# Performance work log

Measured on AMD Instinct MI355X. Metric: run time of the kernel, lower is better.

The kernel has to match this reference:

```python
import jax, jax.numpy as jnp
import numpy as np

B, D, C, T, DEPTH = 4096, 1024, 1000, 32, 6
N_INTERNAL = 2 ** DEPTH - 1
N_LEAVES = 2 ** DEPTH


def setup_inputs() -> dict:
    key = jax.random.key(0)
    k0, k1, k2 = jax.random.split(key, 3)
    x = jax.random.normal(k0, (B, D), jnp.float32)
    split_weights = jax.random.normal(k1, (T, N_INTERNAL, D), jnp.float32) * 0.1
    split_biases = jnp.zeros((T, N_INTERNAL), jnp.float32)
    leaf_logits = jax.random.normal(k2, (T, N_LEAVES, C), jnp.float32) * 0.1
    tree_weights = jnp.ones((T,), jnp.float32) / T
    log_temperature = jnp.zeros((), jnp.float32)
    return {
        "x": x,
        "split_weights": split_weights,
        "split_biases": split_biases,
        "leaf_logits": leaf_logits,
        "tree_weights": tree_weights,
        "log_temperature": log_temperature,
    }


def reference(x, split_weights, split_biases, leaf_logits, tree_weights, log_temperature):
    depth = int(np.log2(leaf_logits.shape[1]))
    temp = jnp.clip(jnp.exp(log_temperature), 0.1, 5.0)
    # split probabilities for all trees at once: [B, T, I]
    logits = jnp.einsum('bd,tid->bti', x, split_weights) + split_biases[None, :, :]
    s = jax.nn.sigmoid(logits / temp)
    b, t, _ = s.shape
    # iterative-doubling path probabilities; BFS leaf order matches the
    # original per-leaf loop (left child multiplies (1-s), right multiplies s)
    mu = jnp.ones((b, t, 1), s.dtype)
    for d in range(depth):
        lvl = s[:, :, 2 ** d - 1: 2 ** (d + 1) - 1]  # [B, T, 2^d] level-d splits
        mu = jnp.stack([mu * (1.0 - lvl), mu * lvl], axis=-1).reshape(b, t, 2 ** (d + 1))
    leaf_class_probs = jax.nn.softmax(leaf_logits / temp, axis=-1)  # [T, L, C]
    w = jax.nn.softmax(tree_weights, axis=0)                        # [T]
    # fused tree-weighted blend, avoids materializing [B, T, C]
    return jnp.einsum('btl,t,tlc->bc', mu, w, leaf_class_probs)
```

## Files before the change

kernel.cpp:

```cpp
#include <hip/hip_runtime.h>
#include <cstdint>
#include <cstddef>

constexpr int Bv = 4096;
constexpr int Dv = 1024;
constexpr int Cv = 1000;
constexpr int Tv = 32;
constexpr int NI = 63;
constexpr int NL = 64;
constexpr int TNp = 2048;
constexpr int TL = Tv * NL;
constexpr int Npad = 1024;

typedef _Float16 h8  __attribute__((ext_vector_type(8)));
typedef _Float16 h4  __attribute__((ext_vector_type(4)));
typedef short    s8v __attribute__((ext_vector_type(8)));
typedef unsigned short us8 __attribute__((ext_vector_type(8)));
typedef float    f4v __attribute__((ext_vector_type(4)));

constexpr size_t N_X    = (size_t)Bv * Dv;
constexpr size_t N_W    = (size_t)TNp * Dv;
constexpr size_t OFF_XH = 64;
constexpr size_t OFF_WH = OFF_XH + N_X / 2;
constexpr size_t OFF_P  = OFF_WH + N_W / 2;
constexpr size_t OFF_MH = OFF_P + (size_t)TL * Cv;
constexpr size_t OFF_PTH= OFF_MH + (size_t)Bv * TL / 2;

__device__ __forceinline__ unsigned short f2bf_rn(float x) {
    unsigned u = __float_as_uint(x);
    return (unsigned short)((u + 0x7fffu + ((u >> 16) & 1u)) >> 16);
}

__device__ __forceinline__ void gll16(const void* gptr, void* lptr) {
    __builtin_amdgcn_global_load_lds(
        (const __attribute__((address_space(1))) unsigned int*)gptr,
        (__attribute__((address_space(3))) unsigned int*)lptr,
        16, 0, 0);
}

__global__ __launch_bounds__(256)
void k_prep(const float* __restrict__ x, const float* __restrict__ sw,
            _Float16* __restrict__ Xh, _Float16* __restrict__ Wh) {
    const int b = blockIdx.x;
    const int tid = threadIdx.x;
    const int nbx = (int)(N_X / 1024);
    if (b < nbx) {
        const size_t i4 = ((size_t)b * 256 + tid) * 4;
        const float4 v = *reinterpret_cast<const float4*>(&x[i4]);
        h4 vh;
        vh[0] = (_Float16)v.x; vh[1] = (_Float16)v.y;
        vh[2] = (_Float16)v.z; vh[3] = (_Float16)v.w;
        *reinterpret_cast<h4*>(&Xh[i4]) = vh;
    } else {
        const size_t d4 = ((size_t)(b - nbx) * 256 + tid) * 4;
        const int row = (int)(d4 >> 10);
        const int col = (int)(d4 & 1023);
        const int t = row >> 6, i = row & 63;
        float4 v = make_float4(0.f, 0.f, 0.f, 0.f);
        if (i < NI)
            v = *reinterpret_cast<const float4*>(&sw[(size_t)(t * NI + i) * Dv + col]);
        h4 vh;
        vh[0] = (_Float16)v.x; vh[1] = (_Float16)v.y;
        vh[2] = (_Float16)v.z; vh[3] = (_Float16)v.w;
        *reinterpret_cast<h4*>(&Wh[d4]) = vh;
    }
}

__global__ __launch_bounds__(256, 2)
void k_gemm1mu(const _Float16* __restrict__ Xh, const _Float16* __restrict__ Wh,
               const float* __restrict__ bias, const float* __restrict__ tw,
               const float* __restrict__ lt, unsigned short* __restrict__ MH) {
    __shared__ __align__(16) char lds[4 * 64 * 65 * 4];

    const int tid = threadIdx.x;
    const int wg  = (blockIdx.x & 7) * 64 + (blockIdx.x >> 3);
    const int blk = wg >> 6;
    const int j   = wg & 63;
    const int bx  = (blk & 3) * 4 + (j & 3);
    const int by  = (blk >> 2) * 16 + (j >> 2);
    const int bm = by * 128, bn = bx * 128;

    const int lane = tid & 63, wv = tid >> 6;
    const int wr = wv >> 1, wc = wv & 1;
    const int lrow = lane & 15, kg = (lane >> 4) * 8;
    const int sr = lane >> 2, sc = (lane & 3) * 8;

    const float temp = fminf(fmaxf(expf(lt[0]), 0.1f), 5.0f);
    const float invT = 1.0f / temp;
    const int mytree = 2 * bx + wc;
    float wm = -3.4e38f;
    #pragma unroll
    for (int t = 0; t < Tv; ++t) wm = fmaxf(wm, tw[t]);
    float wsum = 0.f, wmine = 0.f;
    #pragma unroll
    for (int t = 0; t < Tv; ++t) {
        const float e = expf(tw[t] - wm);
        wsum += e;
        if (t == mytree) wmine = e;
    }
    const float wt = wmine / wsum;

    f4v acc[4][4] = {};

#define STG(bufi, k0)                                                         \
    { _Pragma("unroll")                                                       \
      for (int i_ = 0; i_ < 2; ++i_) {                                        \
        const int ch_  = wv * 2 + i_;                                         \
        const int row_ = ch_ * 16 + sr;                                       \
        gll16(&Xh[(size_t)(bm + row_) * Dv + (k0) + sc],                      \
              lds + (bufi) * 16384 + ch_ * 1024);                             \
        gll16(&Wh[(size_t)(bn + row_) * Dv + (k0) + sc],                      \
              lds + (bufi) * 16384 + 8192 + ch_ * 1024);                      \
      } }

    STG(0, 0);
    for (int t = 0; t < 32; ++t) {
        const int cur = t & 1;
        if (t < 31) {
            STG(cur ^ 1, (t + 1) * 32);
            asm volatile("s_waitcnt vmcnt(4)" ::: "memory");
        } else {
            asm volatile("s_waitcnt vmcnt(0)" ::: "memory");
        }
        __builtin_amdgcn_s_barrier();
        __builtin_amdgcn_sched_barrier(0);

        h8 a[4], b[4];
        #pragma unroll
        for (int mf = 0; mf < 4; ++mf)
            a[mf] = *reinterpret_cast<const h8*>(
                lds + cur * 16384 + (wr * 64 + mf * 16 + lrow) * 64 + kg * 2);
        #pragma unroll
        for (int nf = 0; nf < 4; ++nf)
            b[nf] = *reinterpret_cast<const h8*>(
                lds + cur * 16384 + 8192 + (wc * 64 + nf * 16 + lrow) * 64 + kg * 2);
        #pragma unroll
        for (int mf = 0; mf < 4; ++mf)
            #pragma unroll
            for (int nf = 0; nf < 4; ++nf)
                acc[mf][nf] = __builtin_amdgcn_mfma_f32_16x16x32_f16(a[mf], b[nf], acc[mf][nf], 0, 0, 0);

        __builtin_amdgcn_sched_barrier(0);
        asm volatile("s_waitcnt lgkmcnt(0)" ::: "memory");
        __builtin_amdgcn_s_barrier();
    }
#undef STG

    float* scr = (float*)lds + wv * (64 * 65);
    #pragma unroll
    for (int nf = 0; nf < 4; ++nf) {
        const int colB = nf * 16 + lrow;
        const int gcol = bn + wc * 64 + colB;
        const int ii = gcol & 63;
        const float bv = (ii < NI) ? bias[(gcol >> 6) * NI + ii] : 0.f;
        #pragma unroll
        for (int mf = 0; mf < 4; ++mf) {
            #pragma unroll
            for (int r = 0; r < 4; ++r) {
                const int rowB = mf * 16 + (lane >> 4) * 4 + r;
                const float z = (acc[mf][nf][r] + bv) * invT;
                scr[rowB * 65 + colB] = 1.0f / (1.0f + __expf(-z));
            }
        }
    }
    asm volatile("s_waitcnt lgkmcnt(0)" ::: "memory");

    const float* srow = scr + lane * 65;
    float mu[NL];
    mu[0] = wt;
    #pragma unroll
    for (int d = 0; d < 6; ++d) {
        const int width = 1 << d;
        #pragma unroll
        for (int i = width - 1; i >= 0; --i) {
            const float sv = srow[width - 1 + i];
            const float m  = mu[i];
            mu[2 * i + 1] = m * sv;
            mu[2 * i]     = m * (1.0f - sv);
        }
    }
    const size_t obase = (size_t)(bm + wr * 64 + lane) * TL + (size_t)mytree * 64;
    #pragma unroll
    for (int c = 0; c < 8; ++c) {
        us8 vh;
        #pragma unroll
        for (int jj = 0; jj < 8; ++jj) vh[jj] = f2bf_rn(mu[c * 8 + jj]);
        *reinterpret_cast<us8*>(&MH[obase + c * 8]) = vh;
    }
}

__global__ __launch_bounds__(256)
void k_leafsm(const float* __restrict__ LL, const float* __restrict__ lt,
              float* __restrict__ P) {
    const int r = blockIdx.x;
    const int tid = threadIdx.x;
    const float temp = fminf(fmaxf(expf(lt[0]), 0.1f), 5.0f);
    const float invT = 1.0f / temp;
    const float* row = LL + (size_t)r * Cv;
    float* pr = P + (size_t)r * Cv;
    __shared__ float redm[4];
    __shared__ float reds[4];

    float m = -3.4e38f;
    for (int c = tid; c < Cv; c += 256) m = fmaxf(m, row[c] * invT);
    #pragma unroll
    for (int o = 32; o > 0; o >>= 1) m = fmaxf(m, __shfl_down(m, o));
    if ((tid & 63) == 0) redm[tid >> 6] = m;
    __syncthreads();
    m = fmaxf(fmaxf(redm[0], redm[1]), fmaxf(redm[2], redm[3]));

    float sum = 0.f;
    for (int c = tid; c < Cv; c += 256) {
        const float e = expf(row[c] * invT - m);
        pr[c] = e;
        sum += e;
    }
    #pragma unroll
    for (int o = 32; o > 0; o >>= 1) sum += __shfl_down(sum, o);
    if ((tid & 63) == 0) reds[tid >> 6] = sum;
    __syncthreads();
    sum = reds[0] + reds[1] + reds[2] + reds[3];
    const float rs = 1.0f / sum;
    for (int c = tid; c < Cv; c += 256) pr[c] *= rs;
}

__global__ __launch_bounds__(256)
void k_tp(const float* __restrict__ P, unsigned short* __restrict__ PTH) {
    __shared__ float T[64][65];
    const int k0 = blockIdx.x * 64;
    const int c0 = blockIdx.y * 64;
    const int tid = threadIdx.x;
    #pragma unroll
    for (int i = 0; i < 16; ++i) {
        const int idx = tid + i * 256;
        const int kk = idx >> 6, cc = idx & 63;
        const int c = c0 + cc;
        T[kk][cc] = (c < Cv) ? P[(size_t)(k0 + kk) * Cv + c] : 0.f;
    }
    __syncthreads();
    #pragma unroll
    for (int i = 0; i < 16; ++i) {
        const int idx = tid + i * 256;
        const int cc = idx >> 6, kk = idx & 63;
        PTH[(size_t)(c0 + cc) * TL + k0 + kk] = f2bf_rn(T[kk][cc]);
    }
}

__global__ __launch_bounds__(256, 2)
void k_gemm2(const unsigned short* __restrict__ MH, const unsigned short* __restrict__ PTH,
             float* __restrict__ out) {
    __shared__ unsigned short LA[2][2][128][32];
    __shared__ unsigned short LB[2][2][64][32];

    const int tid  = threadIdx.x;
    const int wg  = (blockIdx.x & 7) * 64 + (blockIdx.x >> 3);
    const int blk = wg >> 6;
    const int j   = wg & 63;
    const int bnt = (blk & 1) * 8 + (j & 7);
    const int bmt = (blk >> 1) * 8 + (j >> 3);
    const int bm = bmt * 128, bn = bnt * 64;

    const int lane = tid & 63;
    const int wv   = tid >> 6;
    const int wr   = wv >> 1;
    const int wc   = wv & 1;
    const int lrow = lane & 15;
    const int kg   = (lane >> 4) * 8;
    const int sr   = lane >> 2;
    const int sc   = (lane & 3) * 8;

    f4v acc[4][2] = {};

#define STAGE2(bufi, k0)                                                          \
    { _Pragma("unroll")                                                           \
      for (int kh_ = 0; kh_ < 2; ++kh_) {                                         \
        _Pragma("unroll")                                                         \
        for (int i_ = 0; i_ < 2; ++i_) {                                          \
          const int ch_  = wv * 2 + i_;                                           \
          const int row_ = ch_ * 16 + sr;                                         \
          gll16(&MH[(size_t)(bm + row_) * TL + (k0) + kh_ * 32 + sc],             \
                (char*)&LA[bufi][kh_][0][0] + ch_ * 1024);                        \
        }                                                                         \
        { const int row_ = wv * 16 + sr;                                          \
          gll16(&PTH[(size_t)(bn + row_) * TL + (k0) + kh_ * 32 + sc],            \
                (char*)&LB[bufi][kh_][0][0] + wv * 1024); }                       \
      } }

    STAGE2(0, 0);
    for (int t = 0; t < 32; ++t) {
        const int cur = t & 1;
        if (t < 31) {
            STAGE2(cur ^ 1, (t + 1) * 64);
            asm volatile("s_waitcnt vmcnt(6)" ::: "memory");
        } else {
            asm volatile("s_waitcnt vmcnt(0)" ::: "memory");
        }
        __builtin_amdgcn_s_barrier();
        __builtin_amdgcn_sched_barrier(0);

        #pragma unroll
        for (int kh = 0; kh < 2; ++kh) {
            s8v a[4], b[2];
            #pragma unroll
            for (int mf = 0; mf < 4; ++mf)
                a[mf] = *reinterpret_cast<const s8v*>(&LA[cur][kh][wr * 64 + mf * 16 + lrow][kg]);
            #pragma unroll
            for (int nf = 0; nf < 2; ++nf)
                b[nf] = *reinterpret_cast<const s8v*>(&LB[cur][kh][wc * 32 + nf * 16 + lrow][kg]);
            #pragma unroll
            for (int mf = 0; mf < 4; ++mf)
                #pragma unroll
                for (int nf = 0; nf < 2; ++nf)
                    acc[mf][nf] = __builtin_amdgcn_mfma_f32_16x16x32_bf16(a[mf], b[nf], acc[mf][nf], 0, 0, 0);
        }

        __builtin_amdgcn_sched_barrier(0);
        asm volatile("s_waitcnt lgkmcnt(0)" ::: "memory");
        __builtin_amdgcn_s_barrier();
    }
#undef STAGE2

    #pragma unroll
    for (int nf = 0; nf < 2; ++nf) {
        const int col = bn + wc * 32 + nf * 16 + lrow;
        if (col >= Cv) continue;
        #pragma unroll
        for (int mf = 0; mf < 4; ++mf) {
            #pragma unroll
            for (int r = 0; r < 4; ++r) {
                const int row = bm + wr * 64 + mf * 16 + (lane >> 4) * 4 + r;
                out[(size_t)row * Cv + col] = acc[mf][nf][r];
            }
        }
    }
}

extern "C" void kernel_launch(void* const* d_in, const int* in_sizes, int n_in,
                              void* d_out, int out_size, void* d_ws, size_t ws_size,
                              hipStream_t stream) {
    const float* x  = (const float*)d_in[0];
    const float* sw = (const float*)d_in[1];
    const float* sb = (const float*)d_in[2];
    const float* ll = (const float*)d_in[3];
    const float* tw = (const float*)d_in[4];
    const float* lt = (const float*)d_in[5];

    float* out  = (float*)d_out;
    float* ws   = (float*)d_ws;
    _Float16* Xh = (_Float16*)(ws + OFF_XH);
    _Float16* Wh = (_Float16*)(ws + OFF_WH);
    float* Pbuf = ws + OFF_P;
    unsigned short* MH  = (unsigned short*)(ws + OFF_MH);
    unsigned short* PTH = (unsigned short*)(ws + OFF_PTH);

    k_prep<<<(int)(N_X / 1024 + N_W / 1024), 256, 0, stream>>>(x, sw, Xh, Wh);
    k_gemm1mu<<<512, 256, 0, stream>>>(Xh, Wh, sb, tw, lt, MH);
    k_leafsm<<<TL, 256, 0, stream>>>(ll, lt, Pbuf);
    k_tp<<<dim3(TL / 64, Npad / 64), 256, 0, stream>>>(Pbuf, PTH);
    k_gemm2<<<512, 256, 0, stream>>>(MH, PTH, out);
}
```

Baseline: 89.33 us.

## Merge leaf softmax into prep and transpose into GEMM1, double GEMM1 k-tile

Leaf softmax blocks are appended to the fp16 conversion kernel, and transpose blocks are appended to the GEMM1 launch as extra workgroups, cutting the launch count from five to three and letting independent work share the GPU. The GEMM1 staging tile is widened from 32 to 64 in K, using 64 KB of double-buffered LDS and half as many barrier iterations. The larger LDS footprint may lower occupancy, and the transpose blocks now carry the GEMM kernel's LDS allocation and launch bounds.

```diff
diff --git a/kernel.cpp b/kernel.cpp
--- a/kernel.cpp
+++ b/kernel.cpp
@@ -39,20 +39,21 @@
 }
 
 __global__ __launch_bounds__(256)
-void k_prep(const float* __restrict__ x, const float* __restrict__ sw,
-            _Float16* __restrict__ Xh, _Float16* __restrict__ Wh) {
+void k_prep_leaf(const float* __restrict__ x, const float* __restrict__ sw,
+                 const float* __restrict__ ll, const float* __restrict__ lt,
+                 _Float16* __restrict__ Xh, _Float16* __restrict__ Wh,
+                 float* __restrict__ P) {
     const int b = blockIdx.x;
     const int tid = threadIdx.x;
-    const int nbx = (int)(N_X / 1024);
-    if (b < nbx) {
+    if (b < 4096) {
         const size_t i4 = ((size_t)b * 256 + tid) * 4;
         const float4 v = *reinterpret_cast<const float4*>(&x[i4]);
         h4 vh;
         vh[0] = (_Float16)v.x; vh[1] = (_Float16)v.y;
         vh[2] = (_Float16)v.z; vh[3] = (_Float16)v.w;
         *reinterpret_cast<h4*>(&Xh[i4]) = vh;
-    } else {
-        const size_t d4 = ((size_t)(b - nbx) * 256 + tid) * 4;
+    } else if (b < 6144) {
+        const size_t d4 = ((size_t)(b - 4096) * 256 + tid) * 4;
         const int row = (int)(d4 >> 10);
         const int col = (int)(d4 & 1023);
         const int t = row >> 6, i = row & 63;
@@ -63,16 +64,70 @@
         vh[0] = (_Float16)v.x; vh[1] = (_Float16)v.y;
         vh[2] = (_Float16)v.z; vh[3] = (_Float16)v.w;
         *reinterpret_cast<h4*>(&Wh[d4]) = vh;
+    } else {
+        const int r = b - 6144;
+        const float temp = fminf(fmaxf(expf(lt[0]), 0.1f), 5.0f);
+        const float invT = 1.0f / temp;
+        const float* row = ll + (size_t)r * Cv;
+        float* pr = P + (size_t)r * Cv;
+        __shared__ float redm[4];
+        __shared__ float reds[4];
+
+        float m = -3.4e38f;
+        for (int c = tid; c < Cv; c += 256) m = fmaxf(m, row[c] * invT);
+        #pragma unroll
+        for (int o = 32; o > 0; o >>= 1) m = fmaxf(m, __shfl_down(m, o));
+        if ((tid & 63) == 0) redm[tid >> 6] = m;
+        __syncthreads();
+        m = fmaxf(fmaxf(redm[0], redm[1]), fmaxf(redm[2], redm[3]));
+
+        float sum = 0.f;
+        for (int c = tid; c < Cv; c += 256) {
+            const float e = expf(row[c] * invT - m);
+            pr[c] = e;
+            sum += e;
+        }
+        #pragma unroll
+        for (int o = 32; o > 0; o >>= 1) sum += __shfl_down(sum, o);
+        if ((tid & 63) == 0) reds[tid >> 6] = sum;
+        __syncthreads();
+        sum = reds[0] + reds[1] + reds[2] + reds[3];
+        const float rs = 1.0f / sum;
+        for (int c = tid; c < Cv; c += 256) pr[c] *= rs;
     }
 }
 
 __global__ __launch_bounds__(256, 2)
-void k_gemm1mu(const _Float16* __restrict__ Xh, const _Float16* __restrict__ Wh,
-               const float* __restrict__ bias, const float* __restrict__ tw,
-               const float* __restrict__ lt, unsigned short* __restrict__ MH) {
+void k_gemm1mu_tp(const _Float16* __restrict__ Xh, const _Float16* __restrict__ Wh,
+                  const float* __restrict__ bias, const float* __restrict__ tw,
+                  const float* __restrict__ lt, const float* __restrict__ P,
+                  unsigned short* __restrict__ MH, unsigned short* __restrict__ PTH) {
     __shared__ __align__(16) char lds[4 * 64 * 65 * 4];
 
     const int tid = threadIdx.x;
+
+    if (blockIdx.x >= 512) {
+        const int tpb = blockIdx.x - 512;
+        const int k0 = (tpb & 31) * 64;
+        const int c0 = (tpb >> 5) * 64;
+        float* T = (float*)lds;
+        #pragma unroll
+        for (int i = 0; i < 16; ++i) {
+            const int idx = tid + i * 256;
+            const int kk = idx >> 6, cc = idx & 63;
+            const int c = c0 + cc;
+            T[kk * 65 + cc] = (c < Cv) ? P[(size_t)(k0 + kk) * Cv + c] : 0.f;
+        }
+        __syncthreads();
+        #pragma unroll
+        for (int i = 0; i < 16; ++i) {
+            const int idx = tid + i * 256;
+            const int cc = idx >> 6, kk = idx & 63;
+            PTH[(size_t)(c0 + cc) * TL + k0 + kk] = f2bf_rn(T[kk * 65 + cc]);
+        }
+        return;
+    }
+
     const int wg  = (blockIdx.x & 7) * 64 + (blockIdx.x >> 3);
     const int blk = wg >> 6;
     const int j   = wg & 63;
@@ -83,7 +138,8 @@
     const int lane = tid & 63, wv = tid >> 6;
     const int wr = wv >> 1, wc = wv & 1;
     const int lrow = lane & 15, kg = (lane >> 4) * 8;
-    const int sr = lane >> 2, sc = (lane & 3) * 8;
+    const int sr = lane >> 3;
+    const int sc = (lane & 7) * 8;
 
     const float temp = fminf(fmaxf(expf(lt[0]), 0.1f), 5.0f);
     const float invT = 1.0f / temp;
@@ -104,41 +160,44 @@
 
 #define STG(bufi, k0)                                                         \
     { _Pragma("unroll")                                                       \
-      for (int i_ = 0; i_ < 2; ++i_) {                                        \
-        const int ch_  = wv * 2 + i_;                                         \
-        const int row_ = ch_ * 16 + sr;                                       \
+      for (int i_ = 0; i_ < 4; ++i_) {                                        \
+        const int ch_  = wv * 4 + i_;                                         \
+        const int row_ = ch_ * 8 + sr;                                        \
         gll16(&Xh[(size_t)(bm + row_) * Dv + (k0) + sc],                      \
-              lds + (bufi) * 16384 + ch_ * 1024);                             \
+              lds + (bufi) * 32768 + ch_ * 1024);                             \
         gll16(&Wh[(size_t)(bn + row_) * Dv + (k0) + sc],                      \
-              lds + (bufi) * 16384 + 8192 + ch_ * 1024);                      \
+              lds + (bufi) * 32768 + 16384 + ch_ * 1024);                     \
       } }
 
     STG(0, 0);
-    for (int t = 0; t < 32; ++t) {
+    for (int t = 0; t < 16; ++t) {
         const int cur = t & 1;
-        if (t < 31) {
-            STG(cur ^ 1, (t + 1) * 32);
-            asm volatile("s_waitcnt vmcnt(4)" ::: "memory");
+        if (t < 15) {
+            STG(cur ^ 1, (t + 1) * 64);
+            asm volatile("s_waitcnt vmcnt(8)" ::: "memory");
         } else {
             asm volatile("s_waitcnt vmcnt(0)" ::: "memory");
         }
         __builtin_amdgcn_s_barrier();
         __builtin_amdgcn_sched_barrier(0);
 
-        h8 a[4], b[4];
-        #pragma unroll
-        for (int mf = 0; mf < 4; ++mf)
-            a[mf] = *reinterpret_cast<const h8*>(
-                lds + cur * 16384 + (wr * 64 + mf * 16 + lrow) * 64 + kg * 2);
-        #pragma unroll
-        for (int nf = 0; nf < 4; ++nf)
-            b[nf] = *reinterpret_cast<const h8*>(
-                lds + cur * 16384 + 8192 + (wc * 64 + nf * 16 + lrow) * 64 + kg * 2);
-        #pragma unroll
-        for (int mf = 0; mf < 4; ++mf)
+        #pragma unroll
+        for (int kh = 0; kh < 2; ++kh) {
+            h8 a[4], b[4];
+            #pragma unroll
+            for (int mf = 0; mf < 4; ++mf)
+                a[mf] = *reinterpret_cast<const h8*>(
+                    lds + cur * 32768 + ((wr * 64 + mf * 16 + lrow) * 64 + kh * 32 + kg) * 2);
             #pragma unroll
             for (int nf = 0; nf < 4; ++nf)
-                acc[mf][nf] = __builtin_amdgcn_mfma_f32_16x16x32_f16(a[mf], b[nf], acc[mf][nf], 0, 0, 0);
+                b[nf] = *reinterpret_cast<const h8*>(
+                    lds + cur * 32768 + 16384 + ((wc * 64 + nf * 16 + lrow) * 64 + kh * 32 + kg) * 2);
+            #pragma unroll
+            for (int mf = 0; mf < 4; ++mf)
+                #pragma unroll
+                for (int nf = 0; nf < 4; ++nf)
+                    acc[mf][nf] = __builtin_amdgcn_mfma_f32_16x16x32_f16(a[mf], b[nf], acc[mf][nf], 0, 0, 0);
+        }
 
         __builtin_amdgcn_sched_barrier(0);
         asm volatile("s_waitcnt lgkmcnt(0)" ::: "memory");
@@ -186,63 +245,6 @@
         #pragma unroll
         for (int jj = 0; jj < 8; ++jj) vh[jj] = f2bf_rn(mu[c * 8 + jj]);
         *reinterpret_cast<us8*>(&MH[obase + c * 8]) = vh;
-    }
-}
-
-__global__ __launch_bounds__(256)
-void k_leafsm(const float* __restrict__ LL, const float* __restrict__ lt,
-              float* __restrict__ P) {
-    const int r = blockIdx.x;
-    const int tid = threadIdx.x;
-    const float temp = fminf(fmaxf(expf(lt[0]), 0.1f), 5.0f);
-    const float invT = 1.0f / temp;
-    const float* row = LL + (size_t)r * Cv;
-    float* pr = P + (size_t)r * Cv;
-    __shared__ float redm[4];
-    __shared__ float reds[4];
-
-    float m = -3.4e38f;
-    for (int c = tid; c < Cv; c += 256) m = fmaxf(m, row[c] * invT);
-    #pragma unroll
-    for (int o = 32; o > 0; o >>= 1) m = fmaxf(m, __shfl_down(m, o));
-    if ((tid & 63) == 0) redm[tid >> 6] = m;
-    __syncthreads();
-    m = fmaxf(fmaxf(redm[0], redm[1]), fmaxf(redm[2], redm[3]));
-
-    float sum = 0.f;
-    for (int c = tid; c < Cv; c += 256) {
-        const float e = expf(row[c] * invT - m);
-        pr[c] = e;
-        sum += e;
-    }
-    #pragma unroll
-    for (int o = 32; o > 0; o >>= 1) sum += __shfl_down(sum, o);
-    if ((tid & 63) == 0) reds[tid >> 6] = sum;
-    __syncthreads();
-    sum = reds[0] + reds[1] + reds[2] + reds[3];
-    const float rs = 1.0f / sum;
-    for (int c = tid; c < Cv; c += 256) pr[c] *= rs;
-}
-
-__global__ __launch_bounds__(256)
-void k_tp(const float* __restrict__ P, unsigned short* __restrict__ PTH) {
-    __shared__ float T[64][65];
-    const int k0 = blockIdx.x * 64;
-    const int c0 = blockIdx.y * 64;
-    const int tid = threadIdx.x;
-    #pragma unroll
-    for (int i = 0; i < 16; ++i) {
-        const int idx = tid + i * 256;
-        const int kk = idx >> 6, cc = idx & 63;
-        const int c = c0 + cc;
-        T[kk][cc] = (c < Cv) ? P[(size_t)(k0 + kk) * Cv + c] : 0.f;
-    }
-    __syncthreads();
-    #pragma unroll
-    for (int i = 0; i < 16; ++i) {
-        const int idx = tid + i * 256;
-        const int cc = idx >> 6, kk = idx & 63;
-        PTH[(size_t)(c0 + cc) * TL + k0 + kk] = f2bf_rn(T[kk][cc]);
     }
 }
 
@@ -353,9 +355,7 @@
     unsigned short* MH  = (unsigned short*)(ws + OFF_MH);
     unsigned short* PTH = (unsigned short*)(ws + OFF_PTH);
 
-    k_prep<<<(int)(N_X / 1024 + N_W / 1024), 256, 0, stream>>>(x, sw, Xh, Wh);
-    k_gemm1mu<<<512, 256, 0, stream>>>(Xh, Wh, sb, tw, lt, MH);
-    k_leafsm<<<TL, 256, 0, stream>>>(ll, lt, Pbuf);
-    k_tp<<<dim3(TL / 64, Npad / 64), 256, 0, stream>>>(Pbuf, PTH);
+    k_prep_leaf<<<8192, 256, 0, stream>>>(x, sw, ll, lt, Xh, Wh, Pbuf);
+    k_gemm1mu_tp<<<1024, 256, 0, stream>>>(Xh, Wh, sb, tw, lt, Pbuf, MH, PTH);
     k_gemm2<<<512, 256, 0, stream>>>(MH, PTH, out);
 }
```

Result: faster. 85.83 us (-3.9%).
